# Kernel optimization log

Measured on AMD Instinct MI355X. Metric: run time of the kernel, lower is better.

The kernel has to match this reference:

```python
import jax, jax.numpy as jnp
import numpy as np

EPS = 1e-12  # torch F.normalize eps

def _l2norm(t):
    # normalize over last axis, matching torch.nn.functional.normalize(dim=-1)
    n = jnp.sqrt(jnp.sum(t * t, axis=-1, keepdims=True))
    return t / jnp.maximum(n, EPS)

def setup_inputs() -> dict:
    key = jax.random.key(0)
    ks = jax.random.split(key, 7)
    b, c, h, w = 8, 192, 128, 128
    num_heads = 6
    x = jax.random.normal(ks[0], (b, c, h, w), dtype=jnp.float32)
    y = jax.random.normal(ks[1], (b, c, h, w), dtype=jnp.float32)
    s = 0.02
    Wq = jax.random.normal(ks[2], (c, c), dtype=jnp.float32) * s
    Wk = jax.random.normal(ks[3], (c, c), dtype=jnp.float32) * s
    Wv = jax.random.normal(ks[4], (c, c), dtype=jnp.float32) * s
    Wo = jax.random.normal(ks[5], (c, c), dtype=jnp.float32) * s
    temperature = jnp.ones((num_heads, 1, 1), dtype=jnp.float32)
    return {"x": x, "y": y, "Wq": Wq, "Wk": Wk, "Wv": Wv, "Wo": Wo,
            "temperature": temperature, "num_heads": num_heads}

def reference(x, y, Wq, Wk, Wv, Wo, temperature, num_heads):
    b, c, h, w = x.shape
    hw = h * w
    ch = c // num_heads
    proj = lambda t, W: jnp.einsum('oc,bchw->bohw', W, t)  # 1x1 conv, no bias
    q = proj(x, Wq).reshape(b, num_heads, ch, hw)
    k = proj(y, Wk).reshape(b, num_heads, ch, hw)
    v = proj(y, Wv).reshape(b, num_heads, ch, hw)
    q = _l2norm(q)
    k = _l2norm(k)
    # channel-wise attention: [b, head, ch, ch]
    attn = jnp.einsum('bhcn,bhdn->bhcd', q, k) * temperature[None]
    attn = jax.nn.softmax(attn, axis=-1)
    out = jnp.einsum('bhcd,bhdn->bhcn', attn, v).reshape(b, c, h, w)
    return proj(out, Wo)
```

## Files before the change

### kernel.cpp

```cpp
#include <hip/hip_runtime.h>
#include <hip/hip_bf16.h>

typedef __bf16 bf16;
typedef bf16 bf16x8 __attribute__((ext_vector_type(8)));
typedef bf16 bf16x4v __attribute__((ext_vector_type(4)));
typedef float f32x4 __attribute__((ext_vector_type(4)));

#define BB 8
#define CC 192
#define NH 6
#define HWN 16384
#define KSPLIT 16
#define KLEN (HWN / KSPLIT)
#define KC 64
#define GSLAB (3 * BB * CC * CC)

__global__ __launch_bounds__(512) void gram_kernel(
    const float* __restrict__ x, const float* __restrict__ y,
    float* __restrict__ dst, int use_atomic)
{
  const int ks = blockIdx.x, b = blockIdx.y, type = blockIdx.z;
  const int tid = threadIdx.x;
  const int lane = tid & 63, w = tid >> 6;
  const int rowbase = (w >> 2) * 96, colbase = (w & 3) * 48;
  const int lo = lane & 15, hi = lane >> 4;

  __shared__ bf16 tileA[CC * KC];
  __shared__ bf16 tileB[CC * KC];

  const float* asrc = (type == 2) ? y : x;
  const bf16* fragB = (type == 0) ? tileB : tileA;

  f32x4 acc[6][3];
  #pragma unroll
  for (int m = 0; m < 6; ++m)
    #pragma unroll
    for (int n = 0; n < 3; ++n) acc[m][n] = (f32x4){0.f, 0.f, 0.f, 0.f};

  const int k0 = ks * KLEN;

  for (int ch = 0; ch < KLEN / KC; ++ch) {
    const int nbase = k0 + ch * KC;
    #pragma unroll
    for (int i = 0; i < 6; ++i) {
      int s = tid + 512 * i;
      int r = s >> 4, c4 = s & 15;
      const float4 v = *(const float4*)(asrc + ((size_t)(b * CC + r)) * HWN + nbase + c4 * 4);
      bf16x4v hv = { (bf16)v.x, (bf16)v.y, (bf16)v.z, (bf16)v.w };
      int byte = (r * (KC * 2) + c4 * 8) ^ ((r & 7) << 4);
      *(bf16x4v*)((char*)tileA + byte) = hv;
    }
    if (type == 0) {
      #pragma unroll
      for (int i = 0; i < 6; ++i) {
        int s = tid + 512 * i;
        int r = s >> 4, c4 = s & 15;
        const float4 v = *(const float4*)(y + ((size_t)(b * CC + r)) * HWN + nbase + c4 * 4);
        bf16x4v hv = { (bf16)v.x, (bf16)v.y, (bf16)v.z, (bf16)v.w };
        int byte = (r * (KC * 2) + c4 * 8) ^ ((r & 7) << 4);
        *(bf16x4v*)((char*)tileB + byte) = hv;
      }
    }
    __syncthreads();

    #pragma unroll
    for (int kk = 0; kk < KC; kk += 32) {
      const int kb = (kk + hi * 8) * 2;
      bf16x8 bfr[3];
      #pragma unroll
      for (int nt = 0; nt < 3; ++nt) {
        int rB = colbase + nt * 16 + lo;
        int byte = (rB * (KC * 2) + kb) ^ ((rB & 7) << 4);
        bfr[nt] = *(const bf16x8*)((const char*)fragB + byte);
      }
      #pragma unroll
      for (int mt = 0; mt < 6; ++mt) {
        int rA = rowbase + mt * 16 + lo;
        int byte = (rA * (KC * 2) + kb) ^ ((rA & 7) << 4);
        bf16x8 afr = *(const bf16x8*)((const char*)tileA + byte);
        #pragma unroll
        for (int nt = 0; nt < 3; ++nt)
          acc[mt][nt] = __builtin_amdgcn_mfma_f32_16x16x32_bf16(afr, bfr[nt], acc[mt][nt], 0, 0, 0);
      }
    }
    __syncthreads();
  }

  if (use_atomic) {
    float* gb = dst + ((size_t)(type * BB + b)) * CC * CC;
    #pragma unroll
    for (int mt = 0; mt < 6; ++mt)
      #pragma unroll
      for (int nt = 0; nt < 3; ++nt)
        #pragma unroll
        for (int r = 0; r < 4; ++r) {
          int rm = rowbase + mt * 16 + hi * 4 + r;
          int cn = colbase + nt * 16 + lo;
          atomicAdd(gb + rm * CC + cn, acc[mt][nt][r]);
        }
  } else {
    float* gb = dst + (size_t)ks * GSLAB + ((size_t)(type * BB + b)) * CC * CC;
    #pragma unroll
    for (int mt = 0; mt < 6; ++mt)
      #pragma unroll
      for (int nt = 0; nt < 3; ++nt)
        #pragma unroll
        for (int r = 0; r < 4; ++r) {
          int rm = rowbase + mt * 16 + hi * 4 + r;
          int cn = colbase + nt * 16 + lo;
          gb[rm * CC + cn] = acc[mt][nt][r];
        }
  }
}

__global__ void reduce_kernel(const float* __restrict__ gpart, float* __restrict__ gram)
{
  const size_t i = (size_t)blockIdx.x * 256 + threadIdx.x;
  float a = 0.f;
  #pragma unroll
  for (int s = 0; s < KSPLIT; ++s) a += gpart[(size_t)s * GSLAB + i];
  gram[i] = a;
}

__global__ void s1_kernel(const float* __restrict__ gram, const float* __restrict__ Wq,
                          const float* __restrict__ Wk, float* __restrict__ tuv)
{
  const int rc = blockIdx.x, b = blockIdx.y, type = blockIdx.z;
  const float* W = (type == 1) ? Wq : Wk;
  const float* G = gram + ((size_t)(type * BB + b)) * CC * CC;
  float* T = tuv + ((size_t)(type * BB + b)) * CC * CC;
  const int d = threadIdx.x;
  const int r0 = rc * 24;
  float acc[24];
  #pragma unroll
  for (int i = 0; i < 24; ++i) acc[i] = 0.f;
  for (int dc = 0; dc < 4; ++dc) {
    float4 w4[12];
    const float4* wp = (const float4*)(W + d * CC + dc * 48);
    #pragma unroll
    for (int j = 0; j < 12; ++j) w4[j] = wp[j];
    for (int ci = 0; ci < 24; ++ci) {
      const float4* g4 = (const float4*)(G + (r0 + ci) * CC + dc * 48);
      float a = acc[ci];
      #pragma unroll
      for (int j = 0; j < 12; ++j) {
        float4 g = g4[j];
        a += g.x * w4[j].x + g.y * w4[j].y + g.z * w4[j].z + g.w * w4[j].w;
      }
      acc[ci] = a;
    }
  }
  #pragma unroll
  for (int ci = 0; ci < 24; ++ci) T[(r0 + ci) * CC + d] = acc[ci];
}

__global__ void s2_kernel(const float* __restrict__ tuv, const float* __restrict__ Wq,
                          const float* __restrict__ Wk, const float* __restrict__ Wv,
                          const float* __restrict__ temperature, float* __restrict__ z)
{
  const int h = blockIdx.x, b = blockIdx.y;
  const int tid = threadIdx.x;
  const float* T  = tuv + ((size_t)(0 * BB + b)) * CC * CC;
  const float* U  = tuv + ((size_t)(1 * BB + b)) * CC * CC;
  const float* V2 = tuv + ((size_t)(2 * BB + b)) * CC * CC;
  __shared__ float sA[32][33];
  __shared__ float snq[32];
  __shared__ float snk[32];

  const int dd = tid & 31, cg = tid >> 5;
  float s[4] = {0.f, 0.f, 0.f, 0.f};
  for (int cp = 0; cp < CC; ++cp) {
    float tv = T[cp * CC + h * 32 + dd];
    #pragma unroll
    for (int i = 0; i < 4; ++i)
      s[i] += Wq[(h * 32 + cg + 8 * i) * CC + cp] * tv;
  }
  if (tid < 32) {
    float a = 0.f;
    for (int cp = 0; cp < CC; ++cp)
      a += Wq[(h * 32 + tid) * CC + cp] * U[cp * CC + h * 32 + tid];
    snq[tid] = fmaxf(sqrtf(fmaxf(a, 0.f)), 1e-12f);
  } else if (tid < 64) {
    int t2 = tid - 32;
    float a = 0.f;
    for (int cp = 0; cp < CC; ++cp)
      a += Wk[(h * 32 + t2) * CC + cp] * V2[cp * CC + h * 32 + t2];
    snk[t2] = fmaxf(sqrtf(fmaxf(a, 0.f)), 1e-12f);
  }
  __syncthreads();

  const float temp = temperature[h];
  const float rk = 1.f / snk[dd];
  #pragma unroll
  for (int i = 0; i < 4; ++i) {
    int ccr = cg + 8 * i;
    float l = s[i] * (1.f / snq[ccr]) * rk * temp;
    float m = l;
    #pragma unroll
    for (int msk = 16; msk >= 1; msk >>= 1) m = fmaxf(m, __shfl_xor(m, msk));
    float p = expf(l - m);
    float su = p;
    #pragma unroll
    for (int msk = 16; msk >= 1; msk >>= 1) su += __shfl_xor(su, msk);
    sA[ccr][dd] = p / su;
  }
  __syncthreads();

  const int c2l = tid & 63, ccg = tid >> 6;
  float za[8][3];
  #pragma unroll
  for (int i = 0; i < 8; ++i)
    #pragma unroll
    for (int j = 0; j < 3; ++j) za[i][j] = 0.f;
  for (int d2 = 0; d2 < 32; ++d2) {
    float wv[3];
    #pragma unroll
    for (int j = 0; j < 3; ++j) wv[j] = Wv[(h * 32 + d2) * CC + c2l + 64 * j];
    #pragma unroll
    for (int i = 0; i < 8; ++i) {
      float a = sA[ccg * 8 + i][d2];
      #pragma unroll
      for (int j = 0; j < 3; ++j) za[i][j] += a * wv[j];
    }
  }
  #pragma unroll
  for (int i = 0; i < 8; ++i)
    #pragma unroll
    for (int j = 0; j < 3; ++j)
      z[((size_t)b * CC + h * 32 + ccg * 8 + i) * CC + c2l + 64 * j] = za[i][j];
}

__global__ void s3_kernel(const float* __restrict__ z, const float* __restrict__ Wo,
                          bf16* __restrict__ pb)
{
  const int oc = blockIdx.x, b = blockIdx.y;
  const int d = threadIdx.x;
  const int o0 = oc * 24;
  const float* Z = z + (size_t)b * CC * CC;
  float acc[24];
  #pragma unroll
  for (int i = 0; i < 24; ++i) acc[i] = 0.f;
  for (int c = 0; c < CC; ++c) {
    float zv = Z[c * CC + d];
    #pragma unroll
    for (int oi = 0; oi < 24; ++oi)
      acc[oi] += Wo[(o0 + oi) * CC + c] * zv;
  }
  bf16* P = pb + (size_t)b * CC * CC;
  #pragma unroll
  for (int oi = 0; oi < 24; ++oi)
    P[(o0 + oi) * CC + d] = (bf16)acc[oi];
}

__global__ __launch_bounds__(256) void f_kernel(const float* __restrict__ y,
                                                const bf16* __restrict__ pb,
                                                float* __restrict__ out)
{
  const int nc = blockIdx.x, b = blockIdx.y;
  const int tid = threadIdx.x;
  const int lane = tid & 63, w = tid >> 6;
  const int lo = lane & 15, hi = lane >> 4;
  const int rowbase = w * 48;
  __shared__ bf16 yt[32][68];

  f32x4 acc[3][4];
  #pragma unroll
  for (int m = 0; m < 3; ++m)
    #pragma unroll
    for (int n = 0; n < 4; ++n) acc[m][n] = (f32x4){0.f, 0.f, 0.f, 0.f};

  const int sd = tid >> 4;
  const int sn = (tid & 15) * 4;

  for (int ks = 0; ks < 6; ++ks) {
    const int d0 = ks * 32;
    __syncthreads();
    #pragma unroll
    for (int p = 0; p < 2; ++p) {
      int d = sd + p * 16;
      const float4 v = *(const float4*)(y + ((size_t)(b * CC + d0 + d)) * HWN + nc * 64 + sn);
      bf16x4v hv = { (bf16)v.x, (bf16)v.y, (bf16)v.z, (bf16)v.w };
      *(bf16x4v*)(&yt[d][sn]) = hv;
    }
    __syncthreads();

    bf16x8 pa[3];
    #pragma unroll
    for (int mt = 0; mt < 3; ++mt)
      pa[mt] = *(const bf16x8*)(pb + ((size_t)(b * CC + rowbase + mt * 16 + lo)) * CC + d0 + hi * 8);

    #pragma unroll
    for (int nt = 0; nt < 4; ++nt) {
      bf16x8 bq;
      #pragma unroll
      for (int j = 0; j < 8; ++j) bq[j] = yt[hi * 8 + j][nt * 16 + lo];
      #pragma unroll
      for (int mt = 0; mt < 3; ++mt)
        acc[mt][nt] = __builtin_amdgcn_mfma_f32_16x16x32_bf16(pa[mt], bq, acc[mt][nt], 0, 0, 0);
    }
  }

  #pragma unroll
  for (int mt = 0; mt < 3; ++mt)
    #pragma unroll
    for (int nt = 0; nt < 4; ++nt)
      #pragma unroll
      for (int r = 0; r < 4; ++r) {
        int o = rowbase + mt * 16 + hi * 4 + r;
        out[((size_t)(b * CC + o)) * HWN + nc * 64 + nt * 16 + lo] = acc[mt][nt][r];
      }
}

extern "C" void kernel_launch(void* const* d_in, const int* in_sizes, int n_in,
                              void* d_out, int out_size, void* d_ws, size_t ws_size,
                              hipStream_t stream)
{
  (void)in_sizes; (void)n_in; (void)out_size;
  const float* x  = (const float*)d_in[0];
  const float* y  = (const float*)d_in[1];
  const float* Wq = (const float*)d_in[2];
  const float* Wk = (const float*)d_in[3];
  const float* Wv = (const float*)d_in[4];
  const float* Wo = (const float*)d_in[5];
  const float* temperature = (const float*)d_in[6];
  float* out = (float*)d_out;

  float* ws = (float*)d_ws;
  const size_t G = (size_t)GSLAB;
  const size_t need_part =
      (KSPLIT * G + G + G + (size_t)BB * CC * CC) * sizeof(float) +
      (size_t)BB * CC * CC * sizeof(bf16);

  float *gram, *tuv, *zbuf;
  bf16* pbuf;
  if (ws_size >= need_part) {
    float* gpart = ws;
    gram = gpart + KSPLIT * G;
    tuv  = gram + G;
    zbuf = tuv + G;
    pbuf = (bf16*)(zbuf + (size_t)BB * CC * CC);
    gram_kernel<<<dim3(KSPLIT, BB, 3), 512, 0, stream>>>(x, y, gpart, 0);
    reduce_kernel<<<GSLAB / 256, 256, 0, stream>>>(gpart, gram);
  } else {
    gram = ws;
    tuv  = gram + G;
    zbuf = tuv + G;
    pbuf = (bf16*)(zbuf + (size_t)BB * CC * CC);
    hipMemsetAsync(gram, 0, G * sizeof(float), stream);
    gram_kernel<<<dim3(KSPLIT, BB, 3), 512, 0, stream>>>(x, y, gram, 1);
  }

  s1_kernel<<<dim3(8, BB, 3), 192, 0, stream>>>(gram, Wq, Wk, tuv);
  s2_kernel<<<dim3(NH, BB), 256, 0, stream>>>(tuv, Wq, Wk, Wv, temperature, zbuf);
  s3_kernel<<<dim3(8, BB), 192, 0, stream>>>(zbuf, Wo, pbuf);
  f_kernel<<<dim3(HWN / 64, BB), 256, 0, stream>>>(y, pbuf, out);
}
```

Measured before the change: 522.5 us.

## Fuse three Gram products into one pass and pre-transpose y for final GEMM

The Gram kernel now loads x and y tiles once per block and computes X·Yᵀ, X·Xᵀ and Y·Yᵀ together. The grid is split over column halves instead of product type, so x and y are each read fewer times from global memory. A new transpose kernel writes y as bf16 in an [n][c] layout, so the final output GEMM can fetch MFMA fragments straight from global memory without an LDS stage. The cost is an extra kernel plus a large bf16 workspace buffer, higher register pressure in the Gram kernel, and redundant X/Y tile loads across the column-half blocks.

```diff
diff --git a/kernel.cpp b/kernel.cpp
--- a/kernel.cpp
+++ b/kernel.cpp
@@ -4,6 +4,7 @@
 typedef __bf16 bf16;
 typedef bf16 bf16x8 __attribute__((ext_vector_type(8)));
 typedef bf16 bf16x4v __attribute__((ext_vector_type(4)));
+typedef bf16 bf16x2 __attribute__((ext_vector_type(2)));
 typedef float f32x4 __attribute__((ext_vector_type(4)));
 
 #define BB 8
@@ -13,29 +14,31 @@
 #define KSPLIT 16
 #define KLEN (HWN / KSPLIT)
 #define KC 64
-#define GSLAB (3 * BB * CC * CC)
-
-__global__ __launch_bounds__(512) void gram_kernel(
+#define GN (3 * BB * CC * CC)
+#define ZN (BB * CC * CC)
+#define YTN ((size_t)BB * HWN * CC)
+
+__global__ __launch_bounds__(512, 2) void gram_kernel(
     const float* __restrict__ x, const float* __restrict__ y,
     float* __restrict__ dst, int use_atomic)
 {
-  const int ks = blockIdx.x, b = blockIdx.y, type = blockIdx.z;
+  const int ks = blockIdx.x, b = blockIdx.y, nh = blockIdx.z;
   const int tid = threadIdx.x;
   const int lane = tid & 63, w = tid >> 6;
-  const int rowbase = (w >> 2) * 96, colbase = (w & 3) * 48;
+  const int rowbase = (w >> 1) * 48;
+  const int colbase = nh * 96 + (w & 1) * 48;
   const int lo = lane & 15, hi = lane >> 4;
 
-  __shared__ bf16 tileA[CC * KC];
-  __shared__ bf16 tileB[CC * KC];
-
-  const float* asrc = (type == 2) ? y : x;
-  const bf16* fragB = (type == 0) ? tileB : tileA;
-
-  f32x4 acc[6][3];
-  #pragma unroll
-  for (int m = 0; m < 6; ++m)
-    #pragma unroll
-    for (int n = 0; n < 3; ++n) acc[m][n] = (f32x4){0.f, 0.f, 0.f, 0.f};
+  __shared__ bf16 tX[CC * KC];
+  __shared__ bf16 tY[CC * KC];
+
+  f32x4 acc[3][3][3];
+  #pragma unroll
+  for (int t3 = 0; t3 < 3; ++t3)
+    #pragma unroll
+    for (int m = 0; m < 3; ++m)
+      #pragma unroll
+      for (int n = 0; n < 3; ++n) acc[t3][m][n] = (f32x4){0.f, 0.f, 0.f, 0.f};
 
   const int k0 = ks * KLEN;
 
@@ -45,70 +48,58 @@
     for (int i = 0; i < 6; ++i) {
       int s = tid + 512 * i;
       int r = s >> 4, c4 = s & 15;
-      const float4 v = *(const float4*)(asrc + ((size_t)(b * CC + r)) * HWN + nbase + c4 * 4);
-      bf16x4v hv = { (bf16)v.x, (bf16)v.y, (bf16)v.z, (bf16)v.w };
-      int byte = (r * (KC * 2) + c4 * 8) ^ ((r & 7) << 4);
-      *(bf16x4v*)((char*)tileA + byte) = hv;
-    }
-    if (type == 0) {
-      #pragma unroll
-      for (int i = 0; i < 6; ++i) {
-        int s = tid + 512 * i;
-        int r = s >> 4, c4 = s & 15;
-        const float4 v = *(const float4*)(y + ((size_t)(b * CC + r)) * HWN + nbase + c4 * 4);
-        bf16x4v hv = { (bf16)v.x, (bf16)v.y, (bf16)v.z, (bf16)v.w };
-        int byte = (r * (KC * 2) + c4 * 8) ^ ((r & 7) << 4);
-        *(bf16x4v*)((char*)tileB + byte) = hv;
-      }
+      size_t goff = ((size_t)(b * CC + r)) * HWN + nbase + c4 * 4;
+      const float4 vx = *(const float4*)(x + goff);
+      const float4 vy = *(const float4*)(y + goff);
+      int byte = (r * 128 + c4 * 8) ^ ((r & 7) << 4);
+      *(bf16x4v*)((char*)tX + byte) = (bf16x4v){(bf16)vx.x, (bf16)vx.y, (bf16)vx.z, (bf16)vx.w};
+      *(bf16x4v*)((char*)tY + byte) = (bf16x4v){(bf16)vy.x, (bf16)vy.y, (bf16)vy.z, (bf16)vy.w};
     }
     __syncthreads();
 
     #pragma unroll
     for (int kk = 0; kk < KC; kk += 32) {
       const int kb = (kk + hi * 8) * 2;
-      bf16x8 bfr[3];
+      bf16x8 aX[3], aY[3], bX[3], bY[3];
+      #pragma unroll
+      for (int mt = 0; mt < 3; ++mt) {
+        int rA = rowbase + mt * 16 + lo;
+        int byte = (rA * 128 + kb) ^ ((rA & 7) << 4);
+        aX[mt] = *(const bf16x8*)((const char*)tX + byte);
+        aY[mt] = *(const bf16x8*)((const char*)tY + byte);
+      }
       #pragma unroll
       for (int nt = 0; nt < 3; ++nt) {
         int rB = colbase + nt * 16 + lo;
-        int byte = (rB * (KC * 2) + kb) ^ ((rB & 7) << 4);
-        bfr[nt] = *(const bf16x8*)((const char*)fragB + byte);
+        int byte = (rB * 128 + kb) ^ ((rB & 7) << 4);
+        bX[nt] = *(const bf16x8*)((const char*)tX + byte);
+        bY[nt] = *(const bf16x8*)((const char*)tY + byte);
       }
       #pragma unroll
-      for (int mt = 0; mt < 6; ++mt) {
-        int rA = rowbase + mt * 16 + lo;
-        int byte = (rA * (KC * 2) + kb) ^ ((rA & 7) << 4);
-        bf16x8 afr = *(const bf16x8*)((const char*)tileA + byte);
+      for (int mt = 0; mt < 3; ++mt)
         #pragma unroll
-        for (int nt = 0; nt < 3; ++nt)
-          acc[mt][nt] = __builtin_amdgcn_mfma_f32_16x16x32_bf16(afr, bfr[nt], acc[mt][nt], 0, 0, 0);
-      }
+        for (int nt = 0; nt < 3; ++nt) {
+          acc[0][mt][nt] = __builtin_amdgcn_mfma_f32_16x16x32_bf16(aX[mt], bY[nt], acc[0][mt][nt], 0, 0, 0);
+          acc[1][mt][nt] = __builtin_amdgcn_mfma_f32_16x16x32_bf16(aX[mt], bX[nt], acc[1][mt][nt], 0, 0, 0);
+          acc[2][mt][nt] = __builtin_amdgcn_mfma_f32_16x16x32_bf16(aY[mt], bY[nt], acc[2][mt][nt], 0, 0, 0);
+        }
     }
     __syncthreads();
   }
 
-  if (use_atomic) {
-    float* gb = dst + ((size_t)(type * BB + b)) * CC * CC;
-    #pragma unroll
-    for (int mt = 0; mt < 6; ++mt)
+  #pragma unroll
+  for (int t3 = 0; t3 < 3; ++t3) {
+    float* gb = dst + (use_atomic ? 0 : (size_t)ks * GN) + ((size_t)(t3 * BB + b)) * CC * CC;
+    #pragma unroll
+    for (int mt = 0; mt < 3; ++mt)
       #pragma unroll
       for (int nt = 0; nt < 3; ++nt)
         #pragma unroll
         for (int r = 0; r < 4; ++r) {
           int rm = rowbase + mt * 16 + hi * 4 + r;
           int cn = colbase + nt * 16 + lo;
-          atomicAdd(gb + rm * CC + cn, acc[mt][nt][r]);
-        }
-  } else {
-    float* gb = dst + (size_t)ks * GSLAB + ((size_t)(type * BB + b)) * CC * CC;
-    #pragma unroll
-    for (int mt = 0; mt < 6; ++mt)
-      #pragma unroll
-      for (int nt = 0; nt < 3; ++nt)
-        #pragma unroll
-        for (int r = 0; r < 4; ++r) {
-          int rm = rowbase + mt * 16 + hi * 4 + r;
-          int cn = colbase + nt * 16 + lo;
-          gb[rm * CC + cn] = acc[mt][nt][r];
+          if (use_atomic) atomicAdd(gb + rm * CC + cn, acc[t3][mt][nt][r]);
+          else            gb[rm * CC + cn] = acc[t3][mt][nt][r];
         }
   }
 }
@@ -118,7 +109,7 @@
   const size_t i = (size_t)blockIdx.x * 256 + threadIdx.x;
   float a = 0.f;
   #pragma unroll
-  for (int s = 0; s < KSPLIT; ++s) a += gpart[(size_t)s * GSLAB + i];
+  for (int s = 0; s < KSPLIT; ++s) a += gpart[(size_t)s * GN + i];
   gram[i] = a;
 }
 
@@ -252,16 +243,89 @@
     P[(o0 + oi) * CC + d] = (bf16)acc[oi];
 }
 
-__global__ __launch_bounds__(256) void f_kernel(const float* __restrict__ y,
-                                                const bf16* __restrict__ pb,
-                                                float* __restrict__ out)
+__global__ __launch_bounds__(256) void tr_kernel(const float* __restrict__ y,
+                                                 bf16* __restrict__ yt)
+{
+  const int nc = blockIdx.x, b = blockIdx.y;
+  const int tid = threadIdx.x;
+  __shared__ bf16 t[CC * 66];
+  #pragma unroll
+  for (int i = 0; i < 12; ++i) {
+    int s = tid + 256 * i;
+    int r = s >> 4, c4 = (s & 15) * 4;
+    const float4 v = *(const float4*)(y + ((size_t)(b * CC + r)) * HWN + nc * 64 + c4);
+    bf16* p = t + r * 66 + c4;
+    *(bf16x2*)(p)     = (bf16x2){(bf16)v.x, (bf16)v.y};
+    *(bf16x2*)(p + 2) = (bf16x2){(bf16)v.z, (bf16)v.w};
+  }
+  __syncthreads();
+  const int n = tid >> 2, seg = tid & 3;
+  bf16* dstrow = yt + ((size_t)b * HWN + nc * 64 + n) * CC + seg * 48;
+  #pragma unroll
+  for (int j8 = 0; j8 < 6; ++j8) {
+    bf16x8 o8;
+    #pragma unroll
+    for (int q = 0; q < 8; ++q) o8[q] = t[(seg * 48 + j8 * 8 + q) * 66 + n];
+    *(bf16x8*)(dstrow + j8 * 8) = o8;
+  }
+}
+
+__global__ __launch_bounds__(256, 4) void f_kernel(const bf16* __restrict__ yt,
+                                                   const bf16* __restrict__ pb,
+                                                   float* __restrict__ out)
 {
   const int nc = blockIdx.x, b = blockIdx.y;
   const int tid = threadIdx.x;
   const int lane = tid & 63, w = tid >> 6;
   const int lo = lane & 15, hi = lane >> 4;
   const int rowbase = w * 48;
-  __shared__ bf16 yt[32][68];
+  const bf16* ytb = yt + ((size_t)b * HWN + nc * 64) * CC;
+  const bf16* pbb = pb + (size_t)b * CC * CC;
+
+  f32x4 acc[3][4];
+  #pragma unroll
+  for (int m = 0; m < 3; ++m)
+    #pragma unroll
+    for (int n = 0; n < 4; ++n) acc[m][n] = (f32x4){0.f, 0.f, 0.f, 0.f};
+
+  #pragma unroll
+  for (int ks = 0; ks < 6; ++ks) {
+    const int d0 = ks * 32 + hi * 8;
+    bf16x8 pa[3], yb[4];
+    #pragma unroll
+    for (int mt = 0; mt < 3; ++mt)
+      pa[mt] = *(const bf16x8*)(pbb + (size_t)(rowbase + mt * 16 + lo) * CC + d0);
+    #pragma unroll
+    for (int nt = 0; nt < 4; ++nt)
+      yb[nt] = *(const bf16x8*)(ytb + (size_t)(nt * 16 + lo) * CC + d0);
+    #pragma unroll
+    for (int mt = 0; mt < 3; ++mt)
+      #pragma unroll
+      for (int nt = 0; nt < 4; ++nt)
+        acc[mt][nt] = __builtin_amdgcn_mfma_f32_16x16x32_bf16(pa[mt], yb[nt], acc[mt][nt], 0, 0, 0);
+  }
+
+  #pragma unroll
+  for (int mt = 0; mt < 3; ++mt)
+    #pragma unroll
+    for (int nt = 0; nt < 4; ++nt)
+      #pragma unroll
+      for (int r = 0; r < 4; ++r) {
+        int o = rowbase + mt * 16 + hi * 4 + r;
+        out[((size_t)(b * CC + o)) * HWN + nc * 64 + nt * 16 + lo] = acc[mt][nt][r];
+      }
+}
+
+__global__ __launch_bounds__(256) void f_fb_kernel(const float* __restrict__ y,
+                                                   const bf16* __restrict__ pb,
+                                                   float* __restrict__ out)
+{
+  const int nc = blockIdx.x, b = blockIdx.y;
+  const int tid = threadIdx.x;
+  const int lane = tid & 63, w = tid >> 6;
+  const int lo = lane & 15, hi = lane >> 4;
+  const int rowbase = w * 48;
+  __shared__ bf16 ytl[32][68];
 
   f32x4 acc[3][4];
   #pragma unroll
@@ -279,8 +343,7 @@
     for (int p = 0; p < 2; ++p) {
       int d = sd + p * 16;
       const float4 v = *(const float4*)(y + ((size_t)(b * CC + d0 + d)) * HWN + nc * 64 + sn);
-      bf16x4v hv = { (bf16)v.x, (bf16)v.y, (bf16)v.z, (bf16)v.w };
-      *(bf16x4v*)(&yt[d][sn]) = hv;
+      *(bf16x4v*)(&ytl[d][sn]) = (bf16x4v){(bf16)v.x, (bf16)v.y, (bf16)v.z, (bf16)v.w};
     }
     __syncthreads();
 
@@ -293,7 +356,7 @@
     for (int nt = 0; nt < 4; ++nt) {
       bf16x8 bq;
       #pragma unroll
-      for (int j = 0; j < 8; ++j) bq[j] = yt[hi * 8 + j][nt * 16 + lo];
+      for (int j = 0; j < 8; ++j) bq[j] = ytl[hi * 8 + j][nt * 16 + lo];
       #pragma unroll
       for (int mt = 0; mt < 3; ++mt)
         acc[mt][nt] = __builtin_amdgcn_mfma_f32_16x16x32_bf16(pa[mt], bq, acc[mt][nt], 0, 0, 0);
@@ -326,32 +389,49 @@
   float* out = (float*)d_out;
 
   float* ws = (float*)d_ws;
-  const size_t G = (size_t)GSLAB;
-  const size_t need_part =
-      (KSPLIT * G + G + G + (size_t)BB * CC * CC) * sizeof(float) +
-      (size_t)BB * CC * CC * sizeof(bf16);
-
-  float *gram, *tuv, *zbuf;
-  bf16* pbuf;
-  if (ws_size >= need_part) {
+  const size_t core_f = (size_t)KSPLIT * GN + GN + GN + ZN;
+  const size_t need1 = core_f * 4 + (size_t)ZN * 2;
+  const size_t need2 = need1 + YTN * 2;
+
+  if (ws_size >= need2) {
     float* gpart = ws;
-    gram = gpart + KSPLIT * G;
-    tuv  = gram + G;
-    zbuf = tuv + G;
-    pbuf = (bf16*)(zbuf + (size_t)BB * CC * CC);
-    gram_kernel<<<dim3(KSPLIT, BB, 3), 512, 0, stream>>>(x, y, gpart, 0);
-    reduce_kernel<<<GSLAB / 256, 256, 0, stream>>>(gpart, gram);
+    float* gram  = gpart + (size_t)KSPLIT * GN;
+    float* tuv   = gram + GN;
+    float* zbuf  = tuv + GN;
+    bf16*  pbuf  = (bf16*)(zbuf + ZN);
+    bf16*  ytb   = (bf16*)((char*)pbuf + (size_t)ZN * 2);
+
+    tr_kernel<<<dim3(HWN / 64, BB), 256, 0, stream>>>(y, ytb);
+    gram_kernel<<<dim3(KSPLIT, BB, 2), 512, 0, stream>>>(x, y, gpart, 0);
+    reduce_kernel<<<GN / 256, 256, 0, stream>>>(gpart, gram);
+    s1_kernel<<<dim3(8, BB, 3), 192, 0, stream>>>(gram, Wq, Wk, tuv);
+    s2_kernel<<<dim3(NH, BB), 256, 0, stream>>>(tuv, Wq, Wk, Wv, temperature, zbuf);
+    s3_kernel<<<dim3(8, BB), 192, 0, stream>>>(zbuf, Wo, pbuf);
+    f_kernel<<<dim3(HWN / 64, BB), 256, 0, stream>>>(ytb, pbuf, out);
+  } else if (ws_size >= need1) {
+    float* gpart = ws;
+    float* gram  = gpart + (size_t)KSPLIT * GN;
+    float* tuv   = gram + GN;
+    float* zbuf  = tuv + GN;
+    bf16*  pbuf  = (bf16*)(zbuf + ZN);
+
+    gram_kernel<<<dim3(KSPLIT, BB, 2), 512, 0, stream>>>(x, y, gpart, 0);
+    reduce_kernel<<<GN / 256, 256, 0, stream>>>(gpart, gram);
+    s1_kernel<<<dim3(8, BB, 3), 192, 0, stream>>>(gram, Wq, Wk, tuv);
+    s2_kernel<<<dim3(NH, BB), 256, 0, stream>>>(tuv, Wq, Wk, Wv, temperature, zbuf);
+    s3_kernel<<<dim3(8, BB), 192, 0, stream>>>(zbuf, Wo, pbuf);
+    f_fb_kernel<<<dim3(HWN / 64, BB), 256, 0, stream>>>(y, pbuf, out);
   } else {
-    gram = ws;
-    tuv  = gram + G;
-    zbuf = tuv + G;
-    pbuf = (bf16*)(zbuf + (size_t)BB * CC * CC);
-    hipMemsetAsync(gram, 0, G * sizeof(float), stream);
-    gram_kernel<<<dim3(KSPLIT, BB, 3), 512, 0, stream>>>(x, y, gram, 1);
-  }
-
-  s1_kernel<<<dim3(8, BB, 3), 192, 0, stream>>>(gram, Wq, Wk, tuv);
-  s2_kernel<<<dim3(NH, BB), 256, 0, stream>>>(tuv, Wq, Wk, Wv, temperature, zbuf);
-  s3_kernel<<<dim3(8, BB), 192, 0, stream>>>(zbuf, Wo, pbuf);
-  f_kernel<<<dim3(HWN / 64, BB), 256, 0, stream>>>(y, pbuf, out);
-}
+    float* gram = ws;
+    float* tuv  = gram + GN;
+    float* zbuf = tuv + GN;
+    bf16*  pbuf = (bf16*)(zbuf + ZN);
+
+    hipMemsetAsync(gram, 0, (size_t)GN * sizeof(float), stream);
+    gram_kernel<<<dim3(KSPLIT, BB, 2), 512, 0, stream>>>(x, y, gram, 1);
+    s1_kernel<<<dim3(8, BB, 3), 192, 0, stream>>>(gram, Wq, Wk, tuv);
+    s2_kernel<<<dim3(NH, BB), 256, 0, stream>>>(tuv, Wq, Wk, Wv, temperature, zbuf);
+    s3_kernel<<<dim3(8, BB), 192, 0, stream>>>(zbuf, Wo, pbuf);
+    f_fb_kernel<<<dim3(HWN / 64, BB), 256, 0, stream>>>(y, pbuf, out);
+  }
+}
```

Measured after the change: 555.9 us. 1.06x slower.
